# Kernel optimization log

Measured on AMD Instinct MI355X. Metric: run time of the kernel, lower is better.

Reference implementation:

```python
import jax, jax.numpy as jnp
import numpy as np

TIME_SCALES = [1, 2, 4]
N = 4            # lcm(time_scales) = num streams
K = 3            # num scales (active slots per step)
S = 7            # sum(time_scales) = total slots
D_HEAD = 128     # d
D = D_HEAD * S   # 896
H = N * K        # 12 heads
IO_DIM = 768
MIX_HID = 3584
B = 4
T = 1024
EPS = 1e-5


def _tables():
    # phase-0 active slots: phase % scale == 0, so slot = cumulative offset of each scale
    offsets = np.cumsum([0] + TIME_SCALES[:-1]).astype(np.int32)  # [K] -> [0,1,3]
    ha = np.empty((N, S), dtype=np.int32)
    streams = np.arange(N)
    so = 0
    for si, s in enumerate(TIME_SCALES):
        alpha = N // s
        for j in range(s):
            ha[:, so + j] = si * N + (streams + alpha * j) % N  # SHARED assignment
        so += s
    active_heads = ha[:, offsets]  # [N, K]
    return jnp.asarray(offsets), jnp.asarray(active_heads)

ACTIVE0, ACTIVE_HEADS = _tables()


def _ln(x, g, b):
    m = jnp.mean(x, axis=-1, keepdims=True)
    v = jnp.var(x, axis=-1, keepdims=True)
    return (x - m) / jnp.sqrt(v + EPS) * g + b


def setup_inputs() -> dict:
    key = jax.random.key(0)
    ks = jax.random.split(key, 8)
    return {
        "x": jax.random.normal(ks[0], (B, T, IO_DIM), jnp.float32),
        "enc_W": jax.random.normal(ks[1], (D, IO_DIM), jnp.float32) * IO_DIM ** -0.5,
        "stream_bias": jax.random.normal(ks[2], (N, D), jnp.float32),
        "ln_mix_g": jnp.ones((D,), jnp.float32),
        "ln_mix_b": jnp.zeros((D,), jnp.float32),
        "W1": jax.random.normal(ks[3], (MIX_HID, D), jnp.float32) * D ** -0.5,
        "b1": jnp.zeros((MIX_HID,), jnp.float32),
        "W2": jax.random.normal(ks[4], (D, MIX_HID), jnp.float32) * MIX_HID ** -0.5,
        "b2": jnp.zeros((D,), jnp.float32),
        "ln_attn_g": jnp.ones((D,), jnp.float32),
        "ln_attn_b": jnp.zeros((D,), jnp.float32),
        "Wq": jax.random.normal(ks[5], (H, D, D_HEAD), jnp.float32) * D_HEAD ** -0.5,
        "Wk": jax.random.normal(ks[6], (H, D, D_HEAD), jnp.float32) * D_HEAD ** -0.5,
        "Wv": jax.random.normal(ks[7], (H, D, D_HEAD), jnp.float32) * D_HEAD ** -0.5,
        "R": 1,
        "is_causal": 1,
    }


def reference(x, enc_W, stream_bias, ln_mix_g, ln_mix_b, W1, b1, W2, b2,
              ln_attn_g, ln_attn_b, Wq, Wk, Wv, R, is_causal):
    # encode: [B,T,io] -> [N,B,T,D]
    base = jnp.einsum('bti,di->btd', x, enc_W)
    z = base[None] + stream_bias[:, None, None, :]
    # mixer residual (dropout=0 -> identity)
    h = _ln(z, ln_mix_g, ln_mix_b)
    h = jax.nn.gelu(jnp.einsum('nbtd,hd->nbth', h, W1) + b1, approximate=False)
    h = jnp.einsum('nbth,dh->nbtd', h, W2) + b2
    z_head = z + h                                           # [N,B,T,D]
    z_slots = z_head.reshape(N, B, T, S, D_HEAD)
    z_active = z_slots[:, :, :, ACTIVE0, :]                  # [N,B,T,K,d]
    # per-stream routed head weights
    Wq_a, Wk_a, Wv_a = Wq[ACTIVE_HEADS], Wk[ACTIVE_HEADS], Wv[ACTIVE_HEADS]  # [N,K,D,d]
    z_attn = _ln(z_head, ln_attn_g, ln_attn_b)               # STREAM scope
    q = jnp.einsum('nbth,nkhd->nbtkd', z_attn, Wq_a)
    k = jnp.einsum('nbth,nkhd->nbtkd', z_attn, Wk_a)
    v = jnp.einsum('nbth,nkhd->nbtkd', z_attn, Wv_a)

    def to_heads(u):  # reproduces torch .permute(1,0,2,3,4).contiguous().view(B,N*K,T,d)
        return jnp.transpose(u, (1, 0, 2, 3, 4)).reshape(B, N * K, T, D_HEAD)

    q, k, v = to_heads(q), to_heads(k), to_heads(v)
    scores = jnp.einsum('bhqd,bhkd->bhqk', q, k) * (D_HEAD ** -0.5)
    if is_causal:
        causal = jnp.tril(jnp.ones((T, T), dtype=bool))
        scores = jnp.where(causal, scores, jnp.finfo(scores.dtype).min)
    attn = jax.nn.softmax(scores, axis=-1)
    out = jnp.einsum('bhqk,bhkd->bhqd', attn, v)             # [B,NK,T,d]
    # reproduces torch .view(B,N,K,T,d).permute(1,0,3,2,4)
    out = jnp.transpose(out.reshape(B, N, K, T, D_HEAD), (1, 0, 3, 2, 4))  # [N,B,T,K,d]
    out = out + z_active
    z_next = z_slots.at[:, :, :, ACTIVE0, :].set(out).reshape(N, B, T, D)
    return z_next
```

## Files before the change

### kernel.cpp

```cpp
#include <hip/hip_runtime.h>
#include <math.h>

#define NSTREAM 4
#define KHEADS  3
#define DH      128
#define DD      896
#define HH      12
#define IO      768
#define MIX     3584
#define BB      4
#define TT      1024
#define BT      4096
#define NBT     16384
#define ZSZ     (NSTREAM*BT*DD)
#define QSZ     (BB*HH*TT*DH)

typedef __attribute__((ext_vector_type(8))) short bf16x8;
typedef __attribute__((ext_vector_type(4))) float f32x4;
typedef unsigned short u16;

__device__ __forceinline__ float gelu_exact(float x){
    return 0.5f * x * (1.0f + erff(x * 0.70710678118654752f));
}
__device__ __forceinline__ void split1(float x, unsigned &hi, unsigned &lo){
    unsigned u = __float_as_uint(x);
    unsigned r = u + 0x7FFFu + ((u >> 16) & 1u);
    hi = r >> 16;
    float hf = __uint_as_float(r & 0xFFFF0000u);
    float l = x - hf;
    lo = __float_as_uint(l) >> 16;
}
__device__ __forceinline__ u16 bf16r(float x){
    unsigned u = __float_as_uint(x);
    return (u16)((u + 0x7FFFu + ((u >> 16) & 1u)) >> 16);
}
__device__ __forceinline__ void pack8(const float4 &f0, const float4 &f1,
                                      uint4 &ph, uint4 &pl){
    unsigned h0,h1,l0,l1;
    split1(f0.x,h0,l0); split1(f0.y,h1,l1); ph.x = h0|(h1<<16); pl.x = l0|(l1<<16);
    split1(f0.z,h0,l0); split1(f0.w,h1,l1); ph.y = h0|(h1<<16); pl.y = l0|(l1<<16);
    split1(f1.x,h0,l0); split1(f1.y,h1,l1); ph.z = h0|(h1<<16); pl.z = l0|(l1<<16);
    split1(f1.z,h0,l0); split1(f1.w,h1,l1); ph.w = h0|(h1<<16); pl.w = l0|(l1<<16);
}
__device__ __forceinline__ bf16x8 as_bf(uint4 v){
    union{uint4 u; bf16x8 b;} x; x.u = v; return x.b;
}

__global__ __launch_bounds__(256)
void rowstats(const float* __restrict__ X, float* __restrict__ st)
{
    const int r = blockIdx.x;
    const float* xp = X + (size_t)r * DD;
    const int tid = threadIdx.x;
    float s = 0.f, sq = 0.f;
    if (tid < 224){
        float4 v = *(const float4*)(xp + tid*4);
        s  = v.x + v.y + v.z + v.w;
        sq = v.x*v.x + v.y*v.y + v.z*v.z + v.w*v.w;
    }
    #pragma unroll
    for (int off = 32; off >= 1; off >>= 1){
        s  += __shfl_down(s,  off);
        sq += __shfl_down(sq, off);
    }
    __shared__ float ps[4], pq[4];
    if ((tid & 63) == 0){ ps[tid>>6] = s; pq[tid>>6] = sq; }
    __syncthreads();
    if (tid == 0){
        s  = ps[0]+ps[1]+ps[2]+ps[3];
        sq = pq[0]+pq[1]+pq[2]+pq[3];
        float mean = s * (1.0f/DD);
        float var  = sq * (1.0f/DD) - mean*mean;
        st[2*r]   = mean;
        st[2*r+1] = rsqrtf(var + 1e-5f);
    }
}

__global__ __launch_bounds__(256)
void gemm_enc(const float* __restrict__ A, const float* __restrict__ Bw,
              float* __restrict__ C, int K, const float* __restrict__ bias)
{
    __shared__ float As[8][128];
    __shared__ float Bs[8][128];
    const int tid = threadIdx.x;
    const int tx = tid & 15, ty = tid >> 4;
    const int m0 = blockIdx.x * 128, n0 = blockIdx.y * 128;
    const int lrow = tid >> 1;
    const int lk   = (tid & 1) * 4;
    const float* Ap = A  + (size_t)(m0 + lrow) * K + lk;
    const float* Bp = Bw + (size_t)(n0 + lrow) * K + lk;

    float acc[8][8];
    #pragma unroll
    for (int i=0;i<8;i++)
        #pragma unroll
        for (int j=0;j<8;j++) acc[i][j] = 0.f;

    for (int k0 = 0; k0 < K; k0 += 8){
        float4 av = *(const float4*)(Ap + k0);
        float4 bv = *(const float4*)(Bp + k0);
        As[lk+0][lrow]=av.x; As[lk+1][lrow]=av.y; As[lk+2][lrow]=av.z; As[lk+3][lrow]=av.w;
        Bs[lk+0][lrow]=bv.x; Bs[lk+1][lrow]=bv.y; Bs[lk+2][lrow]=bv.z; Bs[lk+3][lrow]=bv.w;
        __syncthreads();
        #pragma unroll
        for (int kk = 0; kk < 8; ++kk){
            float a[8], b[8];
            *(float4*)(a)   = *(const float4*)&As[kk][ty*8];
            *(float4*)(a+4) = *(const float4*)&As[kk][ty*8+4];
            *(float4*)(b)   = *(const float4*)&Bs[kk][tx*8];
            *(float4*)(b+4) = *(const float4*)&Bs[kk][tx*8+4];
            #pragma unroll
            for (int i=0;i<8;i++)
                #pragma unroll
                for (int j=0;j<8;j++) acc[i][j] = fmaf(a[i], b[j], acc[i][j]);
        }
        __syncthreads();
    }
    const int rm = m0 + ty*8, rn = n0 + tx*8;
    #pragma unroll
    for (int nn = 0; nn < NSTREAM; ++nn){
        float4 s0 = *(const float4*)(bias + nn*DD + rn);
        float4 s1 = *(const float4*)(bias + nn*DD + rn + 4);
        #pragma unroll
        for (int i=0;i<8;i++){
            float* cp = C + (size_t)(nn*BT + rm + i)*DD + rn;
            float4 o0, o1;
            o0.x=acc[i][0]+s0.x; o0.y=acc[i][1]+s0.y; o0.z=acc[i][2]+s0.z; o0.w=acc[i][3]+s0.w;
            o1.x=acc[i][4]+s1.x; o1.y=acc[i][5]+s1.y; o1.z=acc[i][6]+s1.z; o1.w=acc[i][7]+s1.w;
            *(float4*)cp = o0; *(float4*)(cp+4) = o1;
        }
    }
}

template<int MODE, int MT>
__global__ __launch_bounds__(256, 2)
void mfma_gemm(const float* __restrict__ A, const float* __restrict__ Bw,
               float* __restrict__ C, int K, int ldc,
               const float* __restrict__ stats,
               const float* __restrict__ lng, const float* __restrict__ lnb,
               const float* __restrict__ bias)
{
    constexpr int BM  = 32*MT;
    constexpr int AH  = 0;
    constexpr int ALO = BM*16;
    constexpr int BH  = 2*BM*16;
    constexpr int BLO = BH + 2048;
    __shared__ uint4 smem4[(2*BM*16 + 4096)/4];
    unsigned int* smem = (unsigned int*)smem4;

    const int tid  = threadIdx.x;
    const int lane = tid & 63, wave = tid >> 6;
    const int wm = wave >> 1, wn = wave & 1;
    const int m0 = blockIdx.x * BM, n0 = blockIdx.y * 128;
    const int lr = lane & 15, lc = lane >> 4;

    float meanv[2], rstdv[2];
    if (MODE == 1){
        #pragma unroll
        for (int it = 0; it < MT/2; ++it){
            const int R = (tid + it*256) >> 2;
            meanv[it] = stats[2*(m0+R)];
            rstdv[it] = stats[2*(m0+R)+1];
        }
    }
    f32x4 acc[MT][4];
    #pragma unroll
    for (int mi=0;mi<MT;mi++)
        #pragma unroll
        for (int ni=0;ni<4;ni++) acc[mi][ni] = (f32x4){0.f,0.f,0.f,0.f};

    for (int k0 = 0; k0 < K; k0 += 32){
        __syncthreads();
        #pragma unroll
        for (int it = 0; it < MT/2; ++it){
            const int pos = tid + it*256;
            const int R = pos >> 2, Cc = pos & 3;
            const float* ap = A + (size_t)(m0 + R)*K + k0 + Cc*8;
            float4 f0 = *(const float4*)ap;
            float4 f1 = *(const float4*)(ap + 4);
            if (MODE == 1){
                const float mn = meanv[it], rs = rstdv[it];
                float4 g0 = *(const float4*)(lng + k0 + Cc*8);
                float4 g1 = *(const float4*)(lng + k0 + Cc*8 + 4);
                float4 q0 = *(const float4*)(lnb + k0 + Cc*8);
                float4 q1 = *(const float4*)(lnb + k0 + Cc*8 + 4);
                f0.x=(f0.x-mn)*rs*g0.x+q0.x; f0.y=(f0.y-mn)*rs*g0.y+q0.y;
                f0.z=(f0.z-mn)*rs*g0.z+q0.z; f0.w=(f0.w-mn)*rs*g0.w+q0.w;
                f1.x=(f1.x-mn)*rs*g1.x+q1.x; f1.y=(f1.y-mn)*rs*g1.y+q1.y;
                f1.z=(f1.z-mn)*rs*g1.z+q1.z; f1.w=(f1.w-mn)*rs*g1.w+q1.w;
            }
            uint4 ph, pl; pack8(f0, f1, ph, pl);
            const int ad = R*16 + ((Cc ^ ((R>>1)&3)) << 2);
            *(uint4*)&smem[AH  + ad] = ph;
            *(uint4*)&smem[ALO + ad] = pl;
        }
        #pragma unroll
        for (int it = 0; it < 2; ++it){
            const int pos = tid + it*256;
            const int R = pos >> 2, Cc = pos & 3;
            const float* bp = Bw + (size_t)(n0 + R)*K + k0 + Cc*8;
            float4 f0 = *(const float4*)bp;
            float4 f1 = *(const float4*)(bp + 4);
            uint4 ph, pl; pack8(f0, f1, ph, pl);
            const int ad = R*16 + ((Cc ^ ((R>>1)&3)) << 2);
            *(uint4*)&smem[BH  + ad] = ph;
            *(uint4*)&smem[BLO + ad] = pl;
        }
        __syncthreads();
        bf16x8 ah[MT], al[MT], bh[4], bl[4];
        #pragma unroll
        for (int mi=0; mi<MT; ++mi){
            const int ar = wm*(16*MT) + mi*16 + lr;
            const int ad = ar*16 + ((lc ^ ((ar>>1)&3)) << 2);
            ah[mi] = *reinterpret_cast<const bf16x8*>(&smem[AH  + ad]);
            al[mi] = *reinterpret_cast<const bf16x8*>(&smem[ALO + ad]);
        }
        #pragma unroll
        for (int ni=0; ni<4; ++ni){
            const int br = wn*64 + ni*16 + lr;
            const int ad = br*16 + ((lc ^ ((br>>1)&3)) << 2);
            bh[ni] = *reinterpret_cast<const bf16x8*>(&smem[BH  + ad]);
            bl[ni] = *reinterpret_cast<const bf16x8*>(&smem[BLO + ad]);
        }
        #pragma unroll
        for (int mi=0; mi<MT; ++mi)
            #pragma unroll
            for (int ni=0; ni<4; ++ni){
                acc[mi][ni] = __builtin_amdgcn_mfma_f32_16x16x32_bf16(ah[mi], bh[ni], acc[mi][ni], 0,0,0);
                acc[mi][ni] = __builtin_amdgcn_mfma_f32_16x16x32_bf16(ah[mi], bl[ni], acc[mi][ni], 0,0,0);
                acc[mi][ni] = __builtin_amdgcn_mfma_f32_16x16x32_bf16(al[mi], bh[ni], acc[mi][ni], 0,0,0);
            }
    }
    #pragma unroll
    for (int ni=0; ni<4; ++ni){
        const int col = n0 + wn*64 + ni*16 + lr;
        const float bb = bias[col];
        #pragma unroll
        for (int mi=0; mi<MT; ++mi){
            #pragma unroll
            for (int q=0;q<4;q++){
                const int row = m0 + wm*(16*MT) + mi*16 + lc*4 + q;
                const float v = acc[mi][ni][q] + bb;
                float* cp = C + (size_t)row*ldc + col;
                if (MODE == 1) *cp = gelu_exact(v);
                else           *cp += v;
            }
        }
    }
}

__global__ __launch_bounds__(256)
void wt_split(const float* __restrict__ Wq, const float* __restrict__ Wk,
              const float* __restrict__ Wv, u16* __restrict__ wh, u16* __restrict__ wl)
{
    __shared__ float ftile[32][132];
    const int tid = threadIdx.x;
    const int widx = blockIdx.x, k0 = blockIdx.y*32, which = blockIdx.z;
    const float* W = (which==0 ? Wq : which==1 ? Wk : Wv) + (size_t)widx*DD*DH;
    #pragma unroll
    for (int it=0; it<4; ++it){
        const int pos = tid + it*256;
        const int r = pos >> 5, c4 = (pos & 31)*4;
        float4 v = *(const float4*)(W + (size_t)(k0+r)*DH + c4);
        *(float4*)&ftile[r][c4] = v;
    }
    __syncthreads();
    const int ct = tid >> 1, kseg = (tid & 1)*16;
    unsigned hi[8], lo[8];
    #pragma unroll
    for (int jj=0; jj<8; ++jj){
        unsigned h0,l0,h1,l1;
        split1(ftile[kseg+2*jj  ][ct], h0, l0);
        split1(ftile[kseg+2*jj+1][ct], h1, l1);
        hi[jj] = h0 | (h1<<16);  lo[jj] = l0 | (l1<<16);
    }
    u16* op = wh + ((size_t)((which*12+widx)*128 + ct))*DD + k0 + kseg;
    *(uint4*)op     = make_uint4(hi[0],hi[1],hi[2],hi[3]);
    *(uint4*)(op+8) = make_uint4(hi[4],hi[5],hi[6],hi[7]);
    u16* ol = wl + ((size_t)((which*12+widx)*128 + ct))*DD + k0 + kseg;
    *(uint4*)ol     = make_uint4(lo[0],lo[1],lo[2],lo[3]);
    *(uint4*)(ol+8) = make_uint4(lo[4],lo[5],lo[6],lo[7]);
}

__global__ __launch_bounds__(256, 2)
void qkv_mfma(const float* __restrict__ Z,
              const u16* __restrict__ wh, const u16* __restrict__ wl,
              const float* __restrict__ stats,
              const float* __restrict__ lng, const float* __restrict__ lnb,
              u16* __restrict__ qo, u16* __restrict__ ko, u16* __restrict__ vo)
{
    constexpr int AH = 0, ALO = 2048, BH = 4096, BLO = 6144;
    __shared__ uint4 smem4[8192/4];
    unsigned int* smem = (unsigned int*)smem4;

    const int tid  = threadIdx.x;
    const int lane = tid & 63, wave = tid >> 6;
    const int wm = wave >> 1, wn = wave & 1;
    const int lr = lane & 15, lc = lane >> 4;
    const int m0 = blockIdx.x * 128;
    const int comb = blockIdx.y;
    const int which = comb / 12, widx = comb % 12;
    const int kh = widx >> 2, n = widx & 3;
    const float* Ap = Z + (size_t)n * BT * DD;
    const float* st = stats + (size_t)n * BT * 2;
    const u16* Bh = wh + (size_t)comb * 128 * DD;
    const u16* Bl = wl + (size_t)comb * 128 * DD;
    u16* Op = (which==0 ? qo : which==1 ? ko : vo);

    float meanv[2], rstdv[2];
    #pragma unroll
    for (int it = 0; it < 2; ++it){
        const int R = (tid + it*256) >> 2;
        meanv[it] = st[2*(m0+R)];
        rstdv[it] = st[2*(m0+R)+1];
    }
    f32x4 acc[4][4];
    #pragma unroll
    for (int mi=0;mi<4;mi++)
        #pragma unroll
        for (int ni=0;ni<4;ni++) acc[mi][ni] = (f32x4){0.f,0.f,0.f,0.f};

    for (int k0 = 0; k0 < DD; k0 += 32){
        __syncthreads();
        #pragma unroll
        for (int it = 0; it < 2; ++it){
            const int pos = tid + it*256;
            const int R = pos >> 2, Cc = pos & 3;
            const float* ap = Ap + (size_t)(m0 + R)*DD + k0 + Cc*8;
            float4 f0 = *(const float4*)ap;
            float4 f1 = *(const float4*)(ap + 4);
            const float mn = meanv[it], rs = rstdv[it];
            float4 g0 = *(const float4*)(lng + k0 + Cc*8);
            float4 g1 = *(const float4*)(lng + k0 + Cc*8 + 4);
            float4 q0 = *(const float4*)(lnb + k0 + Cc*8);
            float4 q1 = *(const float4*)(lnb + k0 + Cc*8 + 4);
            f0.x=(f0.x-mn)*rs*g0.x+q0.x; f0.y=(f0.y-mn)*rs*g0.y+q0.y;
            f0.z=(f0.z-mn)*rs*g0.z+q0.z; f0.w=(f0.w-mn)*rs*g0.w+q0.w;
            f1.x=(f1.x-mn)*rs*g1.x+q1.x; f1.y=(f1.y-mn)*rs*g1.y+q1.y;
            f1.z=(f1.z-mn)*rs*g1.z+q1.z; f1.w=(f1.w-mn)*rs*g1.w+q1.w;
            uint4 ph, pl; pack8(f0, f1, ph, pl);
            const int ad = R*16 + ((Cc ^ ((R>>1)&3)) << 2);
            *(uint4*)&smem[AH  + ad] = ph;
            *(uint4*)&smem[ALO + ad] = pl;
        }
        #pragma unroll
        for (int it = 0; it < 2; ++it){
            const int pos = tid + it*256;
            const int R = pos >> 2, Cc = pos & 3;
            const int ad = R*16 + ((Cc ^ ((R>>1)&3)) << 2);
            *(uint4*)&smem[BH  + ad] = *(const uint4*)(Bh + (size_t)R*DD + k0 + Cc*8);
            *(uint4*)&smem[BLO + ad] = *(const uint4*)(Bl + (size_t)R*DD + k0 + Cc*8);
        }
        __syncthreads();
        bf16x8 ah[4], al[4], bh[4], bl[4];
        #pragma unroll
        for (int mi=0; mi<4; ++mi){
            const int ar = wm*64 + mi*16 + lr;
            const int ad = ar*16 + ((lc ^ ((ar>>1)&3)) << 2);
            ah[mi] = *reinterpret_cast<const bf16x8*>(&smem[AH  + ad]);
            al[mi] = *reinterpret_cast<const bf16x8*>(&smem[ALO + ad]);
        }
        #pragma unroll
        for (int ni=0; ni<4; ++ni){
            const int br = wn*64 + ni*16 + lr;
            const int ad = br*16 + ((lc ^ ((br>>1)&3)) << 2);
            bh[ni] = *reinterpret_cast<const bf16x8*>(&smem[BH  + ad]);
            bl[ni] = *reinterpret_cast<const bf16x8*>(&smem[BLO + ad]);
        }
        #pragma unroll
        for (int mi=0; mi<4; ++mi)
            #pragma unroll
            for (int ni=0; ni<4; ++ni){
                acc[mi][ni] = __builtin_amdgcn_mfma_f32_16x16x32_bf16(ah[mi], bh[ni], acc[mi][ni], 0,0,0);
                acc[mi][ni] = __builtin_amdgcn_mfma_f32_16x16x32_bf16(ah[mi], bl[ni], acc[mi][ni], 0,0,0);
                acc[mi][ni] = __builtin_amdgcn_mfma_f32_16x16x32_bf16(al[mi], bh[ni], acc[mi][ni], 0,0,0);
            }
    }
    #pragma unroll
    for (int mi=0; mi<4; ++mi){
        #pragma unroll
        for (int q=0;q<4;q++){
            const int m = m0 + wm*64 + mi*16 + lc*4 + q;
            const int b = m >> 10, t = m & 1023;
            const int v3 = 3*t + kh;
            const int c = v3 >> 10, p = v3 & 1023;
            u16* op = Op + ((size_t)((b*HH + n*KHEADS + c)*TT + p))*DH;
            #pragma unroll
            for (int ni=0; ni<4; ++ni){
                const int col = wn*64 + ni*16 + lr;
                op[col] = bf16r(acc[mi][ni][q]);
            }
        }
    }
}

__global__ __launch_bounds__(256)
void flash_mfma(const u16* __restrict__ qb, const u16* __restrict__ kb,
                const u16* __restrict__ vb, float* __restrict__ Out,
                const int* __restrict__ causal_p)
{
    __shared__ u16 lds[8192 + 8192 + 4608];
    u16* Ks = lds;
    u16* Vt = lds + 8192;
    u16* Pl = lds + 16384;
    const int tid = threadIdx.x, lane = tid & 63, wv = tid >> 6;
    const int lr = lane & 15, lc = lane >> 4;
    const int qt = (int)gridDim.x - 1 - (int)blockIdx.x;
    const int h = blockIdx.y, b = blockIdx.z;
    const int causal = causal_p[0];
    const int n = h / KHEADS, c = h % KHEADS;
    const int s_off = (c == 2 ? 3 : c) * DH;
    const size_t base = (size_t)(b*HH + h) * TT * DH;
    const float scl = 0.08838834764831845f;

    uint4 qf[4];
    const int qrow = qt*64 + wv*16 + lr;
    #pragma unroll
    for (int kc=0; kc<4; ++kc)
        qf[kc] = *(const uint4*)(qb + base + (size_t)qrow*DH + kc*32 + lc*8);

    f32x4 o[8];
    #pragma unroll
    for (int i=0;i<8;i++) o[i] = (f32x4){0.f,0.f,0.f,0.f};
    float mi[4], li[4];
    #pragma unroll
    for (int j=0;j<4;j++){ mi[j] = -1e30f; li[j] = 0.f; }

    const int nkt = causal ? (qt + 1) : 16;
    for (int kt = 0; kt < nkt; ++kt){
        __syncthreads();
        #pragma unroll
        for (int it=0; it<4; ++it){
            const int pos = tid + it*256;
            const int key = pos >> 4, sc = pos & 15;
            uint4 v = *(const uint4*)(kb + base + (size_t)(kt*64+key)*DH + sc*8);
            const int kc = sc >> 2, cc = sc & 3;
            const int word = key*64 + ((kc ^ (key&3))<<4) + ((cc ^ ((key>>2)&3))<<2);
            *(uint4*)(Ks + word*2) = v;
        }
        #pragma unroll
        for (int it=0; it<4; ++it){
            const int pos = tid + it*256;
            const int sc = pos >> 6, key = pos & 63;
            uint4 v = *(const uint4*)(vb + base + (size_t)(kt*64+key)*DH + sc*8);
            const u16* e = (const u16*)&v;
            const int kcv = key>>5, cv = (key>>3)&3, w_ = (key>>1)&3, half = key&1;
            #pragma unroll
            for (int j=0;j<8;++j){
                const int dh = sc*8 + j;
                const int word = dh*32 + ((kcv ^ (dh&1))<<4) + ((cv ^ ((dh>>1)&3))<<2) + w_;
                Vt[word*2 + half] = e[j];
            }
        }
        __syncthreads();
        f32x4 s[4];
        #pragma unroll
        for (int nk=0;nk<4;nk++) s[nk] = (f32x4){0.f,0.f,0.f,0.f};
        #pragma unroll
        for (int kc=0; kc<4; ++kc){
            #pragma unroll
            for (int nk=0; nk<4; ++nk){
                const int key = nk*16 + lr;
                const int word = key*64 + ((kc ^ (key&3))<<4) + ((lc ^ ((key>>2)&3))<<2);
                uint4 kf = *(const uint4*)(Ks + word*2);
                s[nk] = __builtin_amdgcn_mfma_f32_16x16x32_bf16(as_bf(qf[kc]), as_bf(kf), s[nk], 0,0,0);
            }
        }
        #pragma unroll
        for (int nk=0;nk<4;nk++){
            s[nk][0]*=scl; s[nk][1]*=scl; s[nk][2]*=scl; s[nk][3]*=scl;
        }
        if (causal && kt == qt){
            #pragma unroll
            for (int nk=0;nk<4;nk++){
                const int keyg = kt*64 + nk*16 + lr;
                #pragma unroll
                for (int j=0;j<4;j++){
                    const int qg = qt*64 + wv*16 + lc*4 + j;
                    if (keyg > qg) s[nk][j] = -1e30f;
                }
            }
        }
        #pragma unroll
        for (int j=0;j<4;j++){
            float mx = fmaxf(fmaxf(s[0][j], s[1][j]), fmaxf(s[2][j], s[3][j]));
            #pragma unroll
            for (int off=1; off<16; off<<=1) mx = fmaxf(mx, __shfl_xor(mx, off));
            const float mnew = fmaxf(mi[j], mx);
            const float corr = __expf(mi[j] - mnew);
            float p0 = __expf(s[0][j]-mnew), p1 = __expf(s[1][j]-mnew);
            float p2 = __expf(s[2][j]-mnew), p3 = __expf(s[3][j]-mnew);
            float rs = p0+p1+p2+p3;
            #pragma unroll
            for (int off=1; off<16; off<<=1) rs += __shfl_xor(rs, off);
            li[j] = li[j]*corr + rs;
            mi[j] = mnew;
            #pragma unroll
            for (int ni=0;ni<8;ni++) o[ni][j] *= corr;
            const int prow = lc*4 + j;
            u16* pw = Pl + wv*1152 + prow*72;
            pw[lr]      = bf16r(p0);
            pw[16 + lr] = bf16r(p1);
            pw[32 + lr] = bf16r(p2);
            pw[48 + lr] = bf16r(p3);
        }
        uint4 pf[2];
        #pragma unroll
        for (int kc2=0; kc2<2; ++kc2)
            pf[kc2] = *(const uint4*)(Pl + wv*1152 + lr*72 + kc2*32 + lc*8);
        #pragma unroll
        for (int kc2=0; kc2<2; ++kc2){
            #pragma unroll
            for (int ni=0; ni<8; ++ni){
                const int dh = ni*16 + lr;
                const int word = dh*32 + ((kc2 ^ (dh&1))<<4) + ((lc ^ ((dh>>1)&3))<<2);
                uint4 vf = *(const uint4*)(Vt + word*2);
                o[ni] = __builtin_amdgcn_mfma_f32_16x16x32_bf16(as_bf(pf[kc2]), as_bf(vf), o[ni], 0,0,0);
            }
        }
    }
    float inv[4];
    #pragma unroll
    for (int j=0;j<4;j++) inv[j] = 1.0f / li[j];
    #pragma unroll
    for (int j=0;j<4;j++){
        const int p = qt*64 + wv*16 + lc*4 + j;
        float* op = Out + ((size_t)((n*BB + b)*TT + p))*DD + s_off;
        #pragma unroll
        for (int ni=0; ni<8; ++ni)
            op[ni*16 + lr] = o[ni][j] * inv[j];
    }
}

__global__ __launch_bounds__(256)
void assemble(const float* __restrict__ Z, float* __restrict__ out)
{
    const int idx = blockIdx.x * 256 + threadIdx.x;
    const int d4 = idx % 224;
    const size_t loc = (size_t)idx * 4;
    const int s = d4 >> 5;
    float4 v = *(const float4*)(Z + loc);
    if (s == 0 || s == 1 || s == 3){
        const float4 a = *(const float4*)(out + loc);
        v.x += a.x; v.y += a.y; v.z += a.z; v.w += a.w;
    }
    *(float4*)(out + loc) = v;
}

extern "C" void kernel_launch(void* const* d_in, const int* in_sizes, int n_in,
                              void* d_out, int out_size, void* d_ws, size_t ws_size,
                              hipStream_t stream)
{
    (void)in_sizes; (void)n_in; (void)out_size; (void)ws_size;
    const float* x           = (const float*)d_in[0];
    const float* enc_W       = (const float*)d_in[1];
    const float* stream_bias = (const float*)d_in[2];
    const float* ln_mix_g    = (const float*)d_in[3];
    const float* ln_mix_b    = (const float*)d_in[4];
    const float* W1          = (const float*)d_in[5];
    const float* b1          = (const float*)d_in[6];
    const float* W2          = (const float*)d_in[7];
    const float* b2          = (const float*)d_in[8];
    const float* ln_attn_g   = (const float*)d_in[9];
    const float* ln_attn_b   = (const float*)d_in[10];
    const float* Wq          = (const float*)d_in[11];
    const float* Wk          = (const float*)d_in[12];
    const float* Wv          = (const float*)d_in[13];
    const int*   is_causal   = (const int*)d_in[15];
    float* out = (float*)d_out;

    float* z      = (float*)d_ws;
    float* stats  = z + ZSZ;
    float* buf    = stats + NBT*2;
    float* hidden = buf;
    u16*   qbuf   = (u16*)buf;
    u16*   kbuf   = qbuf + QSZ;
    u16*   vbuf   = kbuf + QSZ;
    u16*   wth    = (u16*)(buf + ZSZ);
    u16*   wtl    = wth + 3*HH*DH*DD;

    dim3 blk(256);

    gemm_enc<<<dim3(32, 7), blk, 0, stream>>>(x, enc_W, z, IO, stream_bias);
    wt_split<<<dim3(12, 28, 3), blk, 0, stream>>>(Wq, Wk, Wv, wth, wtl);
    rowstats<<<NBT, blk, 0, stream>>>(z, stats);
    for (int nn = 0; nn < NSTREAM; ++nn){
        mfma_gemm<1,4><<<dim3(32, 28), blk, 0, stream>>>(
            z + (size_t)nn*BT*DD, W1, hidden, DD, MIX,
            stats + (size_t)nn*BT*2, ln_mix_g, ln_mix_b, b1);
        mfma_gemm<2,2><<<dim3(64, 7), blk, 0, stream>>>(
            hidden, W2, z + (size_t)nn*BT*DD, MIX, DD,
            nullptr, nullptr, nullptr, b2);
    }
    rowstats<<<NBT, blk, 0, stream>>>(z, stats);
    qkv_mfma<<<dim3(32, 36), blk, 0, stream>>>(z, wth, wtl, stats,
                                               ln_attn_g, ln_attn_b,
                                               qbuf, kbuf, vbuf);
    flash_mfma<<<dim3(16, HH, BB), blk, 0, stream>>>(qbuf, kbuf, vbuf, out, is_causal);
    assemble<<<ZSZ/4/256, blk, 0, stream>>>(z, out);
}
```

Measured before the change: 1.686 ms.

## Pre-split operands to bf16 hi/lo once and feed GEMMs pre-packed inputs

```diff
diff --git a/kernel.cpp b/kernel.cpp
--- a/kernel.cpp
+++ b/kernel.cpp
@@ -47,14 +47,29 @@
 }
 
 __global__ __launch_bounds__(256)
-void rowstats(const float* __restrict__ X, float* __restrict__ st)
+void split_pair(const float* __restrict__ X, u16* __restrict__ H,
+                u16* __restrict__ L, int n8)
+{
+    const int i = blockIdx.x*256 + threadIdx.x;
+    if (i >= n8) return;
+    float4 f0 = *(const float4*)(X + (size_t)i*8);
+    float4 f1 = *(const float4*)(X + (size_t)i*8 + 4);
+    uint4 ph, pl; pack8(f0, f1, ph, pl);
+    *(uint4*)(H + (size_t)i*8) = ph;
+    *(uint4*)(L + (size_t)i*8) = pl;
+}
+
+__global__ __launch_bounds__(256)
+void ln_split(const float* __restrict__ Z, const float* __restrict__ g,
+              const float* __restrict__ bt, u16* __restrict__ H, u16* __restrict__ L)
 {
     const int r = blockIdx.x;
-    const float* xp = X + (size_t)r * DD;
+    const float* xp = Z + (size_t)r * DD;
     const int tid = threadIdx.x;
+    float4 v = make_float4(0.f,0.f,0.f,0.f);
     float s = 0.f, sq = 0.f;
     if (tid < 224){
-        float4 v = *(const float4*)(xp + tid*4);
+        v = *(const float4*)(xp + tid*4);
         s  = v.x + v.y + v.z + v.w;
         sq = v.x*v.x + v.y*v.y + v.z*v.z + v.w*v.w;
     }
@@ -63,7 +78,7 @@
         s  += __shfl_down(s,  off);
         sq += __shfl_down(sq, off);
     }
-    __shared__ float ps[4], pq[4];
+    __shared__ float ps[4], pq[4], sm, sv;
     if ((tid & 63) == 0){ ps[tid>>6] = s; pq[tid>>6] = sq; }
     __syncthreads();
     if (tid == 0){
@@ -71,80 +86,37 @@
         sq = pq[0]+pq[1]+pq[2]+pq[3];
         float mean = s * (1.0f/DD);
         float var  = sq * (1.0f/DD) - mean*mean;
-        st[2*r]   = mean;
-        st[2*r+1] = rsqrtf(var + 1e-5f);
-    }
-}
-
-__global__ __launch_bounds__(256)
-void gemm_enc(const float* __restrict__ A, const float* __restrict__ Bw,
-              float* __restrict__ C, int K, const float* __restrict__ bias)
-{
-    __shared__ float As[8][128];
-    __shared__ float Bs[8][128];
-    const int tid = threadIdx.x;
-    const int tx = tid & 15, ty = tid >> 4;
-    const int m0 = blockIdx.x * 128, n0 = blockIdx.y * 128;
-    const int lrow = tid >> 1;
-    const int lk   = (tid & 1) * 4;
-    const float* Ap = A  + (size_t)(m0 + lrow) * K + lk;
-    const float* Bp = Bw + (size_t)(n0 + lrow) * K + lk;
-
-    float acc[8][8];
-    #pragma unroll
-    for (int i=0;i<8;i++)
-        #pragma unroll
-        for (int j=0;j<8;j++) acc[i][j] = 0.f;
-
-    for (int k0 = 0; k0 < K; k0 += 8){
-        float4 av = *(const float4*)(Ap + k0);
-        float4 bv = *(const float4*)(Bp + k0);
-        As[lk+0][lrow]=av.x; As[lk+1][lrow]=av.y; As[lk+2][lrow]=av.z; As[lk+3][lrow]=av.w;
-        Bs[lk+0][lrow]=bv.x; Bs[lk+1][lrow]=bv.y; Bs[lk+2][lrow]=bv.z; Bs[lk+3][lrow]=bv.w;
-        __syncthreads();
-        #pragma unroll
-        for (int kk = 0; kk < 8; ++kk){
-            float a[8], b[8];
-            *(float4*)(a)   = *(const float4*)&As[kk][ty*8];
-            *(float4*)(a+4) = *(const float4*)&As[kk][ty*8+4];
-            *(float4*)(b)   = *(const float4*)&Bs[kk][tx*8];
-            *(float4*)(b+4) = *(const float4*)&Bs[kk][tx*8+4];
-            #pragma unroll
-            for (int i=0;i<8;i++)
-                #pragma unroll
-                for (int j=0;j<8;j++) acc[i][j] = fmaf(a[i], b[j], acc[i][j]);
-        }
-        __syncthreads();
-    }
-    const int rm = m0 + ty*8, rn = n0 + tx*8;
-    #pragma unroll
-    for (int nn = 0; nn < NSTREAM; ++nn){
-        float4 s0 = *(const float4*)(bias + nn*DD + rn);
-        float4 s1 = *(const float4*)(bias + nn*DD + rn + 4);
-        #pragma unroll
-        for (int i=0;i<8;i++){
-            float* cp = C + (size_t)(nn*BT + rm + i)*DD + rn;
-            float4 o0, o1;
-            o0.x=acc[i][0]+s0.x; o0.y=acc[i][1]+s0.y; o0.z=acc[i][2]+s0.z; o0.w=acc[i][3]+s0.w;
-            o1.x=acc[i][4]+s1.x; o1.y=acc[i][5]+s1.y; o1.z=acc[i][6]+s1.z; o1.w=acc[i][7]+s1.w;
-            *(float4*)cp = o0; *(float4*)(cp+4) = o1;
-        }
+        sm = mean; sv = rsqrtf(var + 1e-5f);
+    }
+    __syncthreads();
+    if (tid < 224){
+        const float mean = sm, rstd = sv;
+        float4 gg = *(const float4*)(g  + tid*4);
+        float4 bb = *(const float4*)(bt + tid*4);
+        float o0 = (v.x-mean)*rstd*gg.x + bb.x;
+        float o1 = (v.y-mean)*rstd*gg.y + bb.y;
+        float o2 = (v.z-mean)*rstd*gg.z + bb.z;
+        float o3 = (v.w-mean)*rstd*gg.w + bb.w;
+        unsigned h0,l0,h1,l1,h2,l2,h3,l3;
+        split1(o0,h0,l0); split1(o1,h1,l1); split1(o2,h2,l2); split1(o3,h3,l3);
+        *(uint2*)(H + (size_t)r*DD + tid*4) = make_uint2(h0|(h1<<16), h2|(h3<<16));
+        *(uint2*)(L + (size_t)r*DD + tid*4) = make_uint2(l0|(l1<<16), l2|(l3<<16));
     }
 }
 
 template<int MODE, int MT>
 __global__ __launch_bounds__(256, 2)
-void mfma_gemm(const float* __restrict__ A, const float* __restrict__ Bw,
-               float* __restrict__ C, int K, int ldc,
-               const float* __restrict__ stats,
-               const float* __restrict__ lng, const float* __restrict__ lnb,
-               const float* __restrict__ bias)
+void mfma3(const u16* __restrict__ Ah, const u16* __restrict__ Al,
+           const u16* __restrict__ Bh, const u16* __restrict__ Bl,
+           int K, float* __restrict__ C, int ldc,
+           u16* __restrict__ Hh, u16* __restrict__ Hl,
+           const float* __restrict__ bias)
 {
     constexpr int BM  = 32*MT;
-    constexpr int AH  = 0;
-    constexpr int ALO = BM*16;
-    constexpr int BH  = 2*BM*16;
-    constexpr int BLO = BH + 2048;
+    constexpr int AHo = 0;
+    constexpr int ALo = BM*16;
+    constexpr int BHo = 2*BM*16;
+    constexpr int BLo = BHo + 2048;
     __shared__ uint4 smem4[(2*BM*16 + 4096)/4];
     unsigned int* smem = (unsigned int*)smem4;
 
@@ -154,15 +126,6 @@
     const int m0 = blockIdx.x * BM, n0 = blockIdx.y * 128;
     const int lr = lane & 15, lc = lane >> 4;
 
-    float meanv[2], rstdv[2];
-    if (MODE == 1){
-        #pragma unroll
-        for (int it = 0; it < MT/2; ++it){
-            const int R = (tid + it*256) >> 2;
-            meanv[it] = stats[2*(m0+R)];
-            rstdv[it] = stats[2*(m0+R)+1];
-        }
-    }
     f32x4 acc[MT][4];
     #pragma unroll
     for (int mi=0;mi<MT;mi++)
@@ -175,36 +138,19 @@
         for (int it = 0; it < MT/2; ++it){
             const int pos = tid + it*256;
             const int R = pos >> 2, Cc = pos & 3;
-            const float* ap = A + (size_t)(m0 + R)*K + k0 + Cc*8;
-            float4 f0 = *(const float4*)ap;
-            float4 f1 = *(const float4*)(ap + 4);
-            if (MODE == 1){
-                const float mn = meanv[it], rs = rstdv[it];
-                float4 g0 = *(const float4*)(lng + k0 + Cc*8);
-                float4 g1 = *(const float4*)(lng + k0 + Cc*8 + 4);
-                float4 q0 = *(const float4*)(lnb + k0 + Cc*8);
-                float4 q1 = *(const float4*)(lnb + k0 + Cc*8 + 4);
-                f0.x=(f0.x-mn)*rs*g0.x+q0.x; f0.y=(f0.y-mn)*rs*g0.y+q0.y;
-                f0.z=(f0.z-mn)*rs*g0.z+q0.z; f0.w=(f0.w-mn)*rs*g0.w+q0.w;
-                f1.x=(f1.x-mn)*rs*g1.x+q1.x; f1.y=(f1.y-mn)*rs*g1.y+q1.y;
-                f1.z=(f1.z-mn)*rs*g1.z+q1.z; f1.w=(f1.w-mn)*rs*g1.w+q1.w;
-            }
-            uint4 ph, pl; pack8(f0, f1, ph, pl);
             const int ad = R*16 + ((Cc ^ ((R>>1)&3)) << 2);
-            *(uint4*)&smem[AH  + ad] = ph;
-            *(uint4*)&smem[ALO + ad] = pl;
+            const size_t go = (size_t)(m0 + R)*K + k0 + Cc*8;
+            *(uint4*)&smem[AHo + ad] = *(const uint4*)(Ah + go);
+            *(uint4*)&smem[ALo + ad] = *(const uint4*)(Al + go);
         }
         #pragma unroll
         for (int it = 0; it < 2; ++it){
             const int pos = tid + it*256;
             const int R = pos >> 2, Cc = pos & 3;
-            const float* bp = Bw + (size_t)(n0 + R)*K + k0 + Cc*8;
-            float4 f0 = *(const float4*)bp;
-            float4 f1 = *(const float4*)(bp + 4);
-            uint4 ph, pl; pack8(f0, f1, ph, pl);
             const int ad = R*16 + ((Cc ^ ((R>>1)&3)) << 2);
-            *(uint4*)&smem[BH  + ad] = ph;
-            *(uint4*)&smem[BLO + ad] = pl;
+            const size_t go = (size_t)(n0 + R)*K + k0 + Cc*8;
+            *(uint4*)&smem[BHo + ad] = *(const uint4*)(Bh + go);
+            *(uint4*)&smem[BLo + ad] = *(const uint4*)(Bl + go);
         }
         __syncthreads();
         bf16x8 ah[MT], al[MT], bh[4], bl[4];
@@ -212,15 +158,15 @@
         for (int mi=0; mi<MT; ++mi){
             const int ar = wm*(16*MT) + mi*16 + lr;
             const int ad = ar*16 + ((lc ^ ((ar>>1)&3)) << 2);
-            ah[mi] = *reinterpret_cast<const bf16x8*>(&smem[AH  + ad]);
-            al[mi] = *reinterpret_cast<const bf16x8*>(&smem[ALO + ad]);
+            ah[mi] = *reinterpret_cast<const bf16x8*>(&smem[AHo + ad]);
+            al[mi] = *reinterpret_cast<const bf16x8*>(&smem[ALo + ad]);
         }
         #pragma unroll
         for (int ni=0; ni<4; ++ni){
             const int br = wn*64 + ni*16 + lr;
             const int ad = br*16 + ((lc ^ ((br>>1)&3)) << 2);
-            bh[ni] = *reinterpret_cast<const bf16x8*>(&smem[BH  + ad]);
-            bl[ni] = *reinterpret_cast<const bf16x8*>(&smem[BLO + ad]);
+            bh[ni] = *reinterpret_cast<const bf16x8*>(&smem[BHo + ad]);
+            bl[ni] = *reinterpret_cast<const bf16x8*>(&smem[BLo + ad]);
         }
         #pragma unroll
         for (int mi=0; mi<MT; ++mi)
@@ -231,20 +177,50 @@
                 acc[mi][ni] = __builtin_amdgcn_mfma_f32_16x16x32_bf16(al[mi], bh[ni], acc[mi][ni], 0,0,0);
             }
     }
-    #pragma unroll
-    for (int ni=0; ni<4; ++ni){
-        const int col = n0 + wn*64 + ni*16 + lr;
-        const float bb = bias[col];
-        #pragma unroll
-        for (int mi=0; mi<MT; ++mi){
-            #pragma unroll
-            for (int q=0;q<4;q++){
-                const int row = m0 + wm*(16*MT) + mi*16 + lc*4 + q;
-                const float v = acc[mi][ni][q] + bb;
-                float* cp = C + (size_t)row*ldc + col;
-                if (MODE == 1) *cp = gelu_exact(v);
-                else           *cp += v;
-            }
+    if (MODE == 0){
+        #pragma unroll
+        for (int nn = 0; nn < NSTREAM; ++nn){
+            #pragma unroll
+            for (int ni=0; ni<4; ++ni){
+                const int col = n0 + wn*64 + ni*16 + lr;
+                const float sb = bias[nn*DD + col];
+                #pragma unroll
+                for (int mi=0; mi<MT; ++mi)
+                    #pragma unroll
+                    for (int q=0;q<4;q++){
+                        const int row = m0 + wm*(16*MT) + mi*16 + lc*4 + q;
+                        C[(size_t)(nn*BT + row)*ldc + col] = acc[mi][ni][q] + sb;
+                    }
+            }
+        }
+    } else if (MODE == 1){
+        #pragma unroll
+        for (int ni=0; ni<4; ++ni){
+            const int col = n0 + wn*64 + ni*16 + lr;
+            const float bb = bias[col];
+            #pragma unroll
+            for (int mi=0; mi<MT; ++mi)
+                #pragma unroll
+                for (int q=0;q<4;q++){
+                    const int row = m0 + wm*(16*MT) + mi*16 + lc*4 + q;
+                    const float vv = gelu_exact(acc[mi][ni][q] + bb);
+                    unsigned h, l; split1(vv, h, l);
+                    Hh[(size_t)row*ldc + col] = (u16)h;
+                    Hl[(size_t)row*ldc + col] = (u16)l;
+                }
+        }
+    } else {
+        #pragma unroll
+        for (int ni=0; ni<4; ++ni){
+            const int col = n0 + wn*64 + ni*16 + lr;
+            const float bb = bias[col];
+            #pragma unroll
+            for (int mi=0; mi<MT; ++mi)
+                #pragma unroll
+                for (int q=0;q<4;q++){
+                    const int row = m0 + wm*(16*MT) + mi*16 + lc*4 + q;
+                    C[(size_t)row*ldc + col] += acc[mi][ni][q] + bb;
+                }
         }
     }
 }
@@ -283,13 +259,11 @@
 }
 
 __global__ __launch_bounds__(256, 2)
-void qkv_mfma(const float* __restrict__ Z,
-              const u16* __restrict__ wh, const u16* __restrict__ wl,
-              const float* __restrict__ stats,
-              const float* __restrict__ lng, const float* __restrict__ lnb,
-              u16* __restrict__ qo, u16* __restrict__ ko, u16* __restrict__ vo)
-{
-    constexpr int AH = 0, ALO = 2048, BH = 4096, BLO = 6144;
+void qkv3(const u16* __restrict__ zah, const u16* __restrict__ zal,
+          const u16* __restrict__ wh, const u16* __restrict__ wl, int n,
+          u16* __restrict__ qo, u16* __restrict__ ko, u16* __restrict__ vo)
+{
+    constexpr int AHo = 0, ALo = 2048, BHo = 4096, BLo = 6144;
     __shared__ uint4 smem4[8192/4];
     unsigned int* smem = (unsigned int*)smem4;
 
@@ -298,22 +272,11 @@
     const int wm = wave >> 1, wn = wave & 1;
     const int lr = lane & 15, lc = lane >> 4;
     const int m0 = blockIdx.x * 128;
-    const int comb = blockIdx.y;
-    const int which = comb / 12, widx = comb % 12;
-    const int kh = widx >> 2, n = widx & 3;
-    const float* Ap = Z + (size_t)n * BT * DD;
-    const float* st = stats + (size_t)n * BT * 2;
-    const u16* Bh = wh + (size_t)comb * 128 * DD;
-    const u16* Bl = wl + (size_t)comb * 128 * DD;
+    const int which = blockIdx.y / 3, kh = blockIdx.y % 3;
+    const u16* Bh = wh + (size_t)(which*12 + kh*4 + n) * 128 * DD;
+    const u16* Bl = wl + (size_t)(which*12 + kh*4 + n) * 128 * DD;
     u16* Op = (which==0 ? qo : which==1 ? ko : vo);
 
-    float meanv[2], rstdv[2];
-    #pragma unroll
-    for (int it = 0; it < 2; ++it){
-        const int R = (tid + it*256) >> 2;
-        meanv[it] = st[2*(m0+R)];
-        rstdv[it] = st[2*(m0+R)+1];
-    }
     f32x4 acc[4][4];
     #pragma unroll
     for (int mi=0;mi<4;mi++)
@@ -322,34 +285,23 @@
 
     for (int k0 = 0; k0 < DD; k0 += 32){
         __syncthreads();
-        #pragma unroll
-        for (int it = 0; it < 2; ++it){
-            const int pos = tid + it*256;
-            const int R = pos >> 2, Cc = pos & 3;
-            const float* ap = Ap + (size_t)(m0 + R)*DD + k0 + Cc*8;
-            float4 f0 = *(const float4*)ap;
-            float4 f1 = *(const float4*)(ap + 4);
-            const float mn = meanv[it], rs = rstdv[it];
-            float4 g0 = *(const float4*)(lng + k0 + Cc*8);
-            float4 g1 = *(const float4*)(lng + k0 + Cc*8 + 4);
-            float4 q0 = *(const float4*)(lnb + k0 + Cc*8);
-            float4 q1 = *(const float4*)(lnb + k0 + Cc*8 + 4);
-            f0.x=(f0.x-mn)*rs*g0.x+q0.x; f0.y=(f0.y-mn)*rs*g0.y+q0.y;
-            f0.z=(f0.z-mn)*rs*g0.z+q0.z; f0.w=(f0.w-mn)*rs*g0.w+q0.w;
-            f1.x=(f1.x-mn)*rs*g1.x+q1.x; f1.y=(f1.y-mn)*rs*g1.y+q1.y;
-            f1.z=(f1.z-mn)*rs*g1.z+q1.z; f1.w=(f1.w-mn)*rs*g1.w+q1.w;
-            uint4 ph, pl; pack8(f0, f1, ph, pl);
-            const int ad = R*16 + ((Cc ^ ((R>>1)&3)) << 2);
-            *(uint4*)&smem[AH  + ad] = ph;
-            *(uint4*)&smem[ALO + ad] = pl;
-        }
         #pragma unroll
         for (int it = 0; it < 2; ++it){
             const int pos = tid + it*256;
             const int R = pos >> 2, Cc = pos & 3;
             const int ad = R*16 + ((Cc ^ ((R>>1)&3)) << 2);
-            *(uint4*)&smem[BH  + ad] = *(const uint4*)(Bh + (size_t)R*DD + k0 + Cc*8);
-            *(uint4*)&smem[BLO + ad] = *(const uint4*)(Bl + (size_t)R*DD + k0 + Cc*8);
+            const size_t go = (size_t)(m0 + R)*DD + k0 + Cc*8;
+            *(uint4*)&smem[AHo + ad] = *(const uint4*)(zah + go);
+            *(uint4*)&smem[ALo + ad] = *(const uint4*)(zal + go);
+        }
+        #pragma unroll
+        for (int it = 0; it < 2; ++it){
+            const int pos = tid + it*256;
+            const int R = pos >> 2, Cc = pos & 3;
+            const int ad = R*16 + ((Cc ^ ((R>>1)&3)) << 2);
+            const size_t go = (size_t)R*DD + k0 + Cc*8;
+            *(uint4*)&smem[BHo + ad] = *(const uint4*)(Bh + go);
+            *(uint4*)&smem[BLo + ad] = *(const uint4*)(Bl + go);
         }
         __syncthreads();
         bf16x8 ah[4], al[4], bh[4], bl[4];
@@ -357,15 +309,15 @@
         for (int mi=0; mi<4; ++mi){
             const int ar = wm*64 + mi*16 + lr;
             const int ad = ar*16 + ((lc ^ ((ar>>1)&3)) << 2);
-            ah[mi] = *reinterpret_cast<const bf16x8*>(&smem[AH  + ad]);
-            al[mi] = *reinterpret_cast<const bf16x8*>(&smem[ALO + ad]);
+            ah[mi] = *reinterpret_cast<const bf16x8*>(&smem[AHo + ad]);
+            al[mi] = *reinterpret_cast<const bf16x8*>(&smem[ALo + ad]);
         }
         #pragma unroll
         for (int ni=0; ni<4; ++ni){
             const int br = wn*64 + ni*16 + lr;
             const int ad = br*16 + ((lc ^ ((br>>1)&3)) << 2);
-            bh[ni] = *reinterpret_cast<const bf16x8*>(&smem[BH  + ad]);
-            bl[ni] = *reinterpret_cast<const bf16x8*>(&smem[BLO + ad]);
+            bh[ni] = *reinterpret_cast<const bf16x8*>(&smem[BHo + ad]);
+            bl[ni] = *reinterpret_cast<const bf16x8*>(&smem[BLo + ad]);
         }
         #pragma unroll
         for (int mi=0; mi<4; ++mi)
@@ -569,33 +521,54 @@
     const int*   is_causal   = (const int*)d_in[15];
     float* out = (float*)d_out;
 
-    float* z      = (float*)d_ws;
-    float* stats  = z + ZSZ;
-    float* buf    = stats + NBT*2;
-    float* hidden = buf;
-    u16*   qbuf   = (u16*)buf;
-    u16*   kbuf   = qbuf + QSZ;
-    u16*   vbuf   = kbuf + QSZ;
-    u16*   wth    = (u16*)(buf + ZSZ);
-    u16*   wtl    = wth + 3*HH*DH*DD;
-
+    float* z  = (float*)d_ws;
+    u16*   r2 = (u16*)(z + ZSZ);
+    u16* w1h = r2;
+    u16* w1l = r2 + 3211264;
+    u16* w2h = r2 + 6422528;
+    u16* w2l = r2 + 9633792;
+    u16* ahi = r2 + 12845056;
+    u16* alo = r2 + 16516352;
+    u16* hhi = r2 + 20187648;
+    u16* hlo = r2 + 27527680;
+    u16* xh  = r2 + 12845056;
+    u16* xl  = r2 + 15990784;
+    u16* ewh = r2 + 20187648;
+    u16* ewl = r2 + 20875776;
+    u16* wqh = r2;
+    u16* wql = r2 + 4128768;
+    u16* zah = r2 + 8257536;
+    u16* zal = r2 + 11927552;
+    u16* qb  = r2 + 15597568;
+    u16* kb  = r2 + 21889024;
+    u16* vb  = r2 + 28180480;
     dim3 blk(256);
 
-    gemm_enc<<<dim3(32, 7), blk, 0, stream>>>(x, enc_W, z, IO, stream_bias);
-    wt_split<<<dim3(12, 28, 3), blk, 0, stream>>>(Wq, Wk, Wv, wth, wtl);
-    rowstats<<<NBT, blk, 0, stream>>>(z, stats);
+    split_pair<<<1536, blk, 0, stream>>>(x,     xh,  xl,  3145728/8);
+    split_pair<<< 336, blk, 0, stream>>>(enc_W, ewh, ewl,  688128/8);
+    split_pair<<<1568, blk, 0, stream>>>(W1,    w1h, w1l, 3211264/8);
+    split_pair<<<1568, blk, 0, stream>>>(W2,    w2h, w2l, 3211264/8);
+    mfma3<0,4><<<dim3(32, 7), blk, 0, stream>>>(xh, xl, ewh, ewl, IO,
+                                                z, DD, nullptr, nullptr, stream_bias);
     for (int nn = 0; nn < NSTREAM; ++nn){
-        mfma_gemm<1,4><<<dim3(32, 28), blk, 0, stream>>>(
-            z + (size_t)nn*BT*DD, W1, hidden, DD, MIX,
-            stats + (size_t)nn*BT*2, ln_mix_g, ln_mix_b, b1);
-        mfma_gemm<2,2><<<dim3(64, 7), blk, 0, stream>>>(
-            hidden, W2, z + (size_t)nn*BT*DD, MIX, DD,
-            nullptr, nullptr, nullptr, b2);
-    }
-    rowstats<<<NBT, blk, 0, stream>>>(z, stats);
-    qkv_mfma<<<dim3(32, 36), blk, 0, stream>>>(z, wth, wtl, stats,
-                                               ln_attn_g, ln_attn_b,
-                                               qbuf, kbuf, vbuf);
-    flash_mfma<<<dim3(16, HH, BB), blk, 0, stream>>>(qbuf, kbuf, vbuf, out, is_causal);
+        float* zs = z + (size_t)nn*BT*DD;
+        ln_split<<<BT, blk, 0, stream>>>(zs, ln_mix_g, ln_mix_b, ahi, alo);
+        for (int half = 0; half < 2; ++half){
+            const size_t ao = (size_t)half*2048*DD;
+            mfma3<1,4><<<dim3(16, 28), blk, 0, stream>>>(
+                ahi + ao, alo + ao, w1h, w1l, DD,
+                nullptr, MIX, hhi, hlo, b1);
+            mfma3<2,2><<<dim3(32, 7), blk, 0, stream>>>(
+                hhi, hlo, w2h, w2l, MIX,
+                zs + ao, DD, nullptr, nullptr, b2);
+        }
+    }
+    wt_split<<<dim3(12, 28, 3), blk, 0, stream>>>(Wq, Wk, Wv, wqh, wql);
+    for (int nn = 0; nn < NSTREAM; ++nn){
+        ln_split<<<BT, blk, 0, stream>>>(z + (size_t)nn*BT*DD,
+                                         ln_attn_g, ln_attn_b, zah, zal);
+        qkv3<<<dim3(32, 9), blk, 0, stream>>>(zah, zal, wqh, wql, nn, qb, kb, vb);
+    }
+    flash_mfma<<<dim3(16, HH, BB), blk, 0, stream>>>(qb, kb, vb, out, is_causal);
     assemble<<<ZSZ/4/256, blk, 0, stream>>>(z, out);
 }
```

Result: no change. 1.676 ms (-0.6%).
